# Kernel optimization log

Hardware: AMD Instinct MI355X
Metric: run time of the kernel (lower is better)

## Reference

```python
import jax, jax.numpy as jnp
import numpy as np

EPS = 1e-12


def t5_layer_norm(x, w):
    # RMS norm without mean subtraction (T5 style)
    var = jnp.mean(x * x, axis=-1, keepdims=True)
    return w * (x * jax.lax.rsqrt(var + EPS))


def gether(h, a_simi, t_simi, adj):
    # h: [B,S,S,D]; a_simi/t_simi: [B,S]; adj: [B,S,S]
    diag = jnp.einsum('bssd->bsd', h)                 # h[b,l,l,:]
    h_adj = jnp.einsum('bld,blk->blkd', diag, adj)    # diag broadcast by adjacency
    h_y = h * t_simi[:, None, :, None]                # t_simi varies along axis 2
    h_x = h * a_simi[:, :, None, None]                # a_simi varies along axis 1
    h_left = jnp.pad(h_y, ((0, 0), (0, 0), (1, 0), (0, 0)))[:, :, :-1, :]
    h_right = jnp.pad(h_y, ((0, 0), (0, 0), (0, 1), (0, 0)))[:, :, 1:, :]
    h_up = jnp.pad(h_x, ((0, 0), (1, 0), (0, 0), (0, 0)))[:, :-1, :, :]
    h_down = jnp.pad(h_x, ((0, 0), (0, 1), (0, 0), (0, 0)))[:, 1:, :, :]
    return h + h_adj + h_left + h_right + h_up + h_down


def setup_inputs() -> dict:
    key = jax.random.key(0)
    ks = jax.random.split(key, 10)
    B, S, D_in, D_out = 8, 96, 768, 256
    table = jax.random.normal(ks[0], (B, S, S, D_in), dtype=jnp.float32)
    a_simi = jax.random.uniform(ks[1], (B, S), dtype=jnp.float32)
    t_simi = jax.random.uniform(ks[2], (B, S), dtype=jnp.float32)
    adj_matrix = jax.random.uniform(ks[3], (B, S, S), dtype=jnp.float32)
    s1 = 1.0 / np.sqrt(D_in)
    W1 = jax.random.uniform(ks[4], (D_in, D_in), jnp.float32, -s1, s1)
    b1 = jax.random.uniform(ks[5], (D_in,), jnp.float32, -s1, s1)
    g1 = jnp.ones((D_in,), jnp.float32)
    W2 = jax.random.uniform(ks[6], (D_in, D_out), jnp.float32, -s1, s1)
    b2 = jax.random.uniform(ks[7], (D_out,), jnp.float32, -s1, s1)
    g2 = jnp.ones((D_out,), jnp.float32)
    return {"table": table, "a_simi": a_simi, "t_simi": t_simi,
            "adj_matrix": adj_matrix, "W1": W1, "b1": b1, "g1": g1,
            "W2": W2, "b2": b2, "g2": g2}


def reference(table, a_simi, t_simi, adj_matrix, W1, b1, g1, W2, b2, g2):
    h0 = table
    h1 = gether(h0, a_simi, t_simi, adj_matrix)
    h1 = jax.nn.relu(t5_layer_norm((h1 + h0) @ W1 + b1, g1))
    h2 = gether(h1, a_simi, t_simi, adj_matrix)
    h2 = jax.nn.relu(t5_layer_norm((h2 + h1) @ W2 + b2, g2))
    return h2
```

## Files before the change

### kernel.cpp

```cpp
#include <hip/hip_runtime.h>

typedef __bf16 bf16;
typedef __bf16 bf16x4 __attribute__((ext_vector_type(4)));
typedef __bf16 bf16x8 __attribute__((ext_vector_type(8)));
typedef float f32x4 __attribute__((ext_vector_type(4)));
typedef float floatx4 __attribute__((ext_vector_type(4)));

#define S 96
#define DIN 768
#define DOUT 256
#define MROWS 73728

__device__ static inline void async16(const bf16* g, bf16* l) {
    __builtin_amdgcn_global_load_lds(
        (const __attribute__((address_space(1))) void*)g,
        (__attribute__((address_space(3))) void*)l,
        16, 0, 0);
}

__global__ __launch_bounds__(256) void k_cast(
    const float* __restrict__ in, bf16* __restrict__ out, long n)
{
    long i = ((long)blockIdx.x * 256 + threadIdx.x) * 8;
    long stride = (long)gridDim.x * 256 * 8;
    for (; i < n; i += stride) {
        f32x4 a = *(const f32x4*)&in[i];
        f32x4 b = *(const f32x4*)&in[i + 4];
        bf16x8 o;
#pragma unroll
        for (int j = 0; j < 4; ++j) { o[j] = (bf16)a[j]; o[4 + j] = (bf16)b[j]; }
        *(bf16x8*)&out[i] = o;
    }
}

__global__ __launch_bounds__(512, 2) void k_gemm1(
    const bf16* __restrict__ Xm, const bf16* __restrict__ WT,
    bf16* __restrict__ Y)
{
    constexpr int K = 768, N = 768;
    constexpr int NTILE = K / 64;
    __shared__ __align__(16) bf16 As[2][256 * 64];
    __shared__ __align__(16) bf16 Bs[2][256 * 64];
    int t = threadIdx.x;
    int wg = blockIdx.x;
    wg = (wg & 7) * (gridDim.x >> 3) + (wg >> 3);
    int colBase = (wg % 3) * 256;
    int rowBase = (wg / 3) * 256;
    int lane = t & 63, w = t >> 6;
    int quad = lane >> 4, l16 = lane & 15;
    int wr = w >> 2, wc = w & 3;

    floatx4 acc[8][4];
#pragma unroll
    for (int i = 0; i < 8; ++i)
#pragma unroll
        for (int j = 0; j < 4; ++j) acc[i][j] = (floatx4)0.f;

    int tr = t >> 3;
    int gc = (t & 7) ^ (tr & 7);
    const bf16* gA = Xm + (size_t)(rowBase + tr) * K + gc * 8;
    const bf16* gB = WT + (size_t)(colBase + tr) * K + gc * 8;
    int ldst = t * 8;

    auto stageA = [&](int b, int s, int kt) {
        async16(gA + (size_t)s * 64 * K + kt * 64, &As[b][s * 4096 + ldst]);
    };
    auto stageB = [&](int b, int s, int kt) {
        async16(gB + (size_t)s * 64 * K + kt * 64, &Bs[b][s * 4096 + ldst]);
    };

    stageB(0, 0, 0); stageB(0, 1, 0); stageB(0, 2, 0); stageB(0, 3, 0);
    stageA(0, 0, 0); stageA(0, 2, 0); stageA(0, 1, 0); stageA(0, 3, 0);
    asm volatile("s_waitcnt vmcnt(2)" ::: "memory");
    __builtin_amdgcn_s_barrier();

    int swz = l16 & 7;
    int cK0 = (quad ^ swz) * 8;
    int cK1 = ((quad + 4) ^ swz) * 8;

    for (int tt = 0; tt < NTILE; ++tt) {
        int cur = tt & 1;
        int nb = cur ^ 1;
        bool more = (tt + 1 < NTILE);
        const bf16* aB = &As[cur][(wr * 128 + l16) * 64];
        const bf16* bB = &Bs[cur][(wc * 64 + l16) * 64];
#pragma unroll
        for (int p = 0; p < 4; ++p) {
            const int ihalf = p & 1;
            const int co = (p >> 1) ? cK1 : cK0;
            bf16x8 af[4], bfr[4];
#pragma unroll
            for (int ii = 0; ii < 4; ++ii)
                af[ii] = *(const bf16x8*)(aB + (ihalf * 4 + ii) * 1024 + co);
#pragma unroll
            for (int j = 0; j < 4; ++j)
                bfr[j] = *(const bf16x8*)(bB + j * 1024 + co);
            if (more) {
                if (p == 0) { stageB(nb, 0, tt + 1); stageB(nb, 1, tt + 1); }
                if (p == 1) { stageB(nb, 2, tt + 1); stageB(nb, 3, tt + 1); }
                if (p == 2) { stageA(nb, 0, tt + 1); stageA(nb, 2, tt + 1); }
                if (p == 3) { stageA(nb, 1, tt + 1); stageA(nb, 3, tt + 1); }
            }
            __builtin_amdgcn_s_barrier();
            asm volatile("s_waitcnt lgkmcnt(0)" ::: "memory");
            __builtin_amdgcn_sched_barrier(0);
            __builtin_amdgcn_s_setprio(1);
#pragma unroll
            for (int ii = 0; ii < 4; ++ii)
#pragma unroll
                for (int j = 0; j < 4; ++j)
                    acc[ihalf * 4 + ii][j] = __builtin_amdgcn_mfma_f32_16x16x32_bf16(
                        af[ii], bfr[j], acc[ihalf * 4 + ii][j], 0, 0, 0);
            __builtin_amdgcn_s_setprio(0);
            if (p == 0) {
                if (more) asm volatile("s_waitcnt vmcnt(2)" ::: "memory");
                else      asm volatile("s_waitcnt vmcnt(0)" ::: "memory");
            }
            if (p == 3 && more) asm volatile("s_waitcnt vmcnt(2)" ::: "memory");
            __builtin_amdgcn_s_barrier();
        }
    }

#pragma unroll
    for (int i = 0; i < 8; ++i) {
#pragma unroll
        for (int r = 0; r < 4; ++r) {
            int row = rowBase + wr * 128 + i * 16 + quad * 4 + r;
            bf16* yp = Y + (size_t)row * N + colBase + wc * 64 + l16;
#pragma unroll
            for (int j = 0; j < 4; ++j)
                yp[j * 16] = (bf16)acc[i][j][r];
        }
    }
}

__global__ __launch_bounds__(256) void k_gn1(
    const bf16* __restrict__ P, const float* __restrict__ G1,
    const float* __restrict__ B1, const float* __restrict__ Asim,
    const float* __restrict__ Tsim, const float* __restrict__ Adj,
    bf16* __restrict__ O)
{
    __shared__ float adjs[S];
    __shared__ float ts[S];
    __shared__ float diagf[DIN];
    __shared__ float g1s[DIN];
    __shared__ float b1s[DIN];
    int bx = blockIdx.x;
    bx = (bx & 7) * (gridDim.x >> 3) + (bx >> 3);
    int b = bx / S, l = bx % S;
    int tid = threadIdx.x;
    long row0 = (long)(b * S + l) * S;
    for (int i = tid; i < DIN; i += 256) { g1s[i] = G1[i]; b1s[i] = B1[i]; }
    if (tid < S) {
        adjs[tid] = Adj[(b * S + l) * S + tid];
        ts[tid]   = Tsim[b * S + tid];
        bf16x8 dv = *(const bf16x8*)&P[(row0 + l) * DIN + tid * 8];
#pragma unroll
        for (int j = 0; j < 8; ++j) diagf[tid * 8 + j] = (float)dv[j];
    }
    float a_up = (l > 0)     ? Asim[b * S + l - 1] : 0.f;
    float a_dn = (l < S - 1) ? Asim[b * S + l + 1] : 0.f;
    long du = (l > 0)     ? -(long)S * DIN : 0;
    long dd = (l < S - 1) ?  (long)S * DIN : 0;
    __syncthreads();

    int lane = tid & 63, wv = tid >> 6;
    int k0 = blockIdx.y * (S / 2);
    for (int k = k0 + wv; k < k0 + S / 2; k += 4) {
        float tl = (k > 0)     ? ts[k - 1] : 0.f;
        float tr = (k < S - 1) ? ts[k + 1] : 0.f;
        long  dl = (k > 0)     ? -(long)DIN : 0;
        long  dr = (k < S - 1) ?  (long)DIN : 0;
        float aj = adjs[k];
        const bf16* prow = P + (row0 + k) * DIN;
        bf16* orow = O + (row0 + k) * DIN;
        float v[12];
        float ss = 0.f;
        {
            int col = lane * 8;
            const bf16* pc = prow + col;
            bf16x8 vc = *(const bf16x8*)pc;
            bf16x8 vl = *(const bf16x8*)(pc + dl);
            bf16x8 vr = *(const bf16x8*)(pc + dr);
            bf16x8 vu = *(const bf16x8*)(pc + du);
            bf16x8 vd = *(const bf16x8*)(pc + dd);
#pragma unroll
            for (int j = 0; j < 8; ++j) {
                float x = 2.f * (float)vc[j] + aj * diagf[col + j]
                        + tl * (float)vl[j] + tr * (float)vr[j]
                        + a_up * (float)vu[j] + a_dn * (float)vd[j]
                        + b1s[col + j];
                v[j] = x;
                ss += x * x;
            }
        }
        {
            int col = 512 + lane * 4;
            const bf16* pc = prow + col;
            bf16x4 vc = *(const bf16x4*)pc;
            bf16x4 vl = *(const bf16x4*)(pc + dl);
            bf16x4 vr = *(const bf16x4*)(pc + dr);
            bf16x4 vu = *(const bf16x4*)(pc + du);
            bf16x4 vd = *(const bf16x4*)(pc + dd);
#pragma unroll
            for (int j = 0; j < 4; ++j) {
                float x = 2.f * (float)vc[j] + aj * diagf[col + j]
                        + tl * (float)vl[j] + tr * (float)vr[j]
                        + a_up * (float)vu[j] + a_dn * (float)vd[j]
                        + b1s[col + j];
                v[8 + j] = x;
                ss += x * x;
            }
        }
        ss += __shfl_xor(ss, 1);
        ss += __shfl_xor(ss, 2);
        ss += __shfl_xor(ss, 4);
        ss += __shfl_xor(ss, 8);
        ss += __shfl_xor(ss, 16);
        ss += __shfl_xor(ss, 32);
        float inv = rsqrtf(ss * (1.f / DIN) + 1e-12f);
        {
            int col = lane * 8;
            bf16x8 o;
#pragma unroll
            for (int j = 0; j < 8; ++j) {
                float y = v[j] * g1s[col + j] * inv;
                o[j] = (bf16)(y > 0.f ? y : 0.f);
            }
            *(bf16x8*)&orow[col] = o;
        }
        {
            int col = 512 + lane * 4;
            bf16x4 o;
#pragma unroll
            for (int j = 0; j < 4; ++j) {
                float y = v[8 + j] * g1s[col + j] * inv;
                o[j] = (bf16)(y > 0.f ? y : 0.f);
            }
            *(bf16x4*)&orow[col] = o;
        }
    }
}

__global__ __launch_bounds__(256, 2) void k_gemm2(
    const bf16* __restrict__ Xm, const bf16* __restrict__ WT,
    bf16* __restrict__ Y)
{
    constexpr int K = 768, N = 256;
    constexpr int NT = K / 32;
    __shared__ __align__(16) bf16 As[3][128 * 32];
    __shared__ __align__(16) bf16 Bs[3][256 * 32];
    int t = threadIdx.x;
    int rowBase = blockIdx.x * 128;
    int lane = t & 63, w = t >> 6;
    int quad = lane >> 4, l16 = lane & 15;
    int wr = w >> 1, wc = w & 1;

    floatx4 acc[4][8];
#pragma unroll
    for (int i = 0; i < 4; ++i)
#pragma unroll
        for (int j = 0; j < 8; ++j) acc[i][j] = (floatx4)0.f;

    int chunk = (t & 3) ^ ((t >> 3) & 3);
    const bf16* gA = Xm + (size_t)(rowBase + (t >> 2)) * K + chunk * 8;
    const bf16* gB = WT + (size_t)(t >> 2) * K + chunk * 8;
    int l8 = t * 8;

    auto stage = [&](int buf, int kk) {
        async16(gA + kk, &As[buf][l8]);
        async16(gA + kk + 64 * K, &As[buf][l8 + 2048]);
        async16(gB + kk, &Bs[buf][l8]);
        async16(gB + kk + 64 * K, &Bs[buf][l8 + 2048]);
        async16(gB + kk + 128 * K, &Bs[buf][l8 + 4096]);
        async16(gB + kk + 192 * K, &Bs[buf][l8 + 6144]);
    };

    stage(0, 0);
    stage(1, 32);
    for (int tt = 0; tt < NT; ++tt) {
        if (tt + 1 < NT) asm volatile("s_waitcnt vmcnt(6)" ::: "memory");
        else             asm volatile("s_waitcnt vmcnt(0)" ::: "memory");
        __builtin_amdgcn_s_barrier();
        int cur = tt % 3;
        bf16x8 af[4], bfr[8];
#pragma unroll
        for (int i = 0; i < 4; ++i) {
            int ra = wr * 64 + i * 16 + l16;
            af[i] = *(const bf16x8*)&As[cur][ra * 32 + (quad ^ ((ra >> 1) & 3)) * 8];
        }
#pragma unroll
        for (int j = 0; j < 8; ++j) {
            int rb = wc * 128 + j * 16 + l16;
            bfr[j] = *(const bf16x8*)&Bs[cur][rb * 32 + (quad ^ ((rb >> 1) & 3)) * 8];
        }
        if (tt + 2 < NT) stage((tt + 2) % 3, (tt + 2) * 32);
#pragma unroll
        for (int i = 0; i < 4; ++i)
#pragma unroll
            for (int j = 0; j < 8; ++j)
                acc[i][j] = __builtin_amdgcn_mfma_f32_16x16x32_bf16(
                    af[i], bfr[j], acc[i][j], 0, 0, 0);
    }

#pragma unroll
    for (int i = 0; i < 4; ++i) {
#pragma unroll
        for (int r = 0; r < 4; ++r) {
            int row = rowBase + wr * 64 + i * 16 + quad * 4 + r;
            bf16* yp = Y + (size_t)row * N + wc * 128 + l16;
#pragma unroll
            for (int j = 0; j < 8; ++j)
                yp[j * 16] = (bf16)acc[i][j][r];
        }
    }
}

__global__ __launch_bounds__(256) void k_gn2(
    const bf16* __restrict__ P, const float* __restrict__ G2,
    const float* __restrict__ B2, const float* __restrict__ Asim,
    const float* __restrict__ Tsim, const float* __restrict__ Adj,
    float* __restrict__ O)
{
    __shared__ float adjs[S];
    __shared__ float ts[S];
    __shared__ float diagf[DOUT];
    __shared__ float g2s[DOUT];
    __shared__ float b2s[DOUT];
    int bx = blockIdx.x;
    bx = (bx & 7) * (gridDim.x >> 3) + (bx >> 3);
    int b = bx / S, l = bx % S;
    int tid = threadIdx.x;
    long row0 = (long)(b * S + l) * S;
    if (tid < DOUT) { g2s[tid] = G2[tid]; b2s[tid] = B2[tid]; }
    if (tid < S) {
        adjs[tid] = Adj[(b * S + l) * S + tid];
        ts[tid]   = Tsim[b * S + tid];
    }
    if (tid < 32) {
        bf16x8 dv = *(const bf16x8*)&P[(row0 + l) * DOUT + tid * 8];
#pragma unroll
        for (int j = 0; j < 8; ++j) diagf[tid * 8 + j] = (float)dv[j];
    }
    float a_up = (l > 0)     ? Asim[b * S + l - 1] : 0.f;
    float a_dn = (l < S - 1) ? Asim[b * S + l + 1] : 0.f;
    long du = (l > 0)     ? -(long)S * DOUT : 0;
    long dd = (l < S - 1) ?  (long)S * DOUT : 0;
    __syncthreads();

    int lane = tid & 63, wv = tid >> 6;
    int k0 = blockIdx.y * (S / 2);
    for (int k = k0 + wv; k < k0 + S / 2; k += 4) {
        float tl = (k > 0)     ? ts[k - 1] : 0.f;
        float tr = (k < S - 1) ? ts[k + 1] : 0.f;
        long  dl = (k > 0)     ? -(long)DOUT : 0;
        long  dr = (k < S - 1) ?  (long)DOUT : 0;
        float aj = adjs[k];
        const bf16* prow = P + (row0 + k) * DOUT;
        float* orow = O + (row0 + k) * DOUT;
        int col = lane * 4;
        const bf16* pc = prow + col;
        bf16x4 vc = *(const bf16x4*)pc;
        bf16x4 vl = *(const bf16x4*)(pc + dl);
        bf16x4 vr = *(const bf16x4*)(pc + dr);
        bf16x4 vu = *(const bf16x4*)(pc + du);
        bf16x4 vd = *(const bf16x4*)(pc + dd);
        float v[4];
        float ss = 0.f;
#pragma unroll
        for (int j = 0; j < 4; ++j) {
            float x = 2.f * (float)vc[j] + aj * diagf[col + j]
                    + tl * (float)vl[j] + tr * (float)vr[j]
                    + a_up * (float)vu[j] + a_dn * (float)vd[j]
                    + b2s[col + j];
            v[j] = x;
            ss += x * x;
        }
        ss += __shfl_xor(ss, 1);
        ss += __shfl_xor(ss, 2);
        ss += __shfl_xor(ss, 4);
        ss += __shfl_xor(ss, 8);
        ss += __shfl_xor(ss, 16);
        ss += __shfl_xor(ss, 32);
        float inv = rsqrtf(ss * (1.f / DOUT) + 1e-12f);
        f32x4 o;
#pragma unroll
        for (int j = 0; j < 4; ++j) {
            float y = v[j] * g2s[col + j] * inv;
            o[j] = y > 0.f ? y : 0.f;
        }
        *(f32x4*)&orow[col] = o;
    }
}

__global__ __launch_bounds__(256) void k_castT(
    const float* __restrict__ in, bf16* __restrict__ out, int R, int C)
{
    __shared__ float tile[32][33];
    int lx = threadIdx.x & 31, ly = threadIdx.x >> 5;
    int c0 = blockIdx.x * 32, r0 = blockIdx.y * 32;
#pragma unroll
    for (int k = 0; k < 4; ++k)
        tile[ly + 8 * k][lx] = in[(size_t)(r0 + ly + 8 * k) * C + c0 + lx];
    __syncthreads();
#pragma unroll
    for (int k = 0; k < 4; ++k)
        out[(size_t)(c0 + ly + 8 * k) * R + r0 + lx] = (bf16)tile[lx][ly + 8 * k];
}

extern "C" void kernel_launch(void* const* d_in, const int* in_sizes, int n_in,
                              void* d_out, int out_size, void* d_ws, size_t ws_size,
                              hipStream_t stream)
{
    const float* table = (const float*)d_in[0];
    const float* asim  = (const float*)d_in[1];
    const float* tsim  = (const float*)d_in[2];
    const float* adj   = (const float*)d_in[3];
    const float* W1    = (const float*)d_in[4];
    const float* b1    = (const float*)d_in[5];
    const float* g1    = (const float*)d_in[6];
    const float* W2    = (const float*)d_in[7];
    const float* b2    = (const float*)d_in[8];
    const float* g2    = (const float*)d_in[9];
    float* out = (float*)d_out;

    char* ws = (char*)d_ws;
    const size_t SZ_X = (size_t)MROWS * DIN * 2;
    bf16*  A    = (bf16*)ws;
    bf16*  Bb   = (bf16*)(ws + SZ_X);
    bf16*  W1T  = (bf16*)(ws + 2 * SZ_X);
    bf16*  W2T  = (bf16*)(ws + 2 * SZ_X + 1179648);

    k_castT<<<dim3(DIN / 32, DIN / 32), 256, 0, stream>>>(W1, W1T, DIN, DIN);
    k_castT<<<dim3(DOUT / 32, DIN / 32), 256, 0, stream>>>(W2, W2T, DIN, DOUT);

    k_cast<<<2048, 256, 0, stream>>>(table, A, (long)MROWS * DIN);
    k_gemm1<<<dim3((DIN / 256) * (MROWS / 256)), 512, 0, stream>>>(A, W1T, Bb);
    k_gn1<<<dim3(8 * S, 2), 256, 0, stream>>>(Bb, g1, b1, asim, tsim, adj, A);
    k_gemm2<<<MROWS / 128, 256, 0, stream>>>(A, W2T, Bb);
    k_gn2<<<dim3(8 * S, 2), 256, 0, stream>>>(Bb, g2, b2, asim, tsim, adj, out);
}
```

Measured before the change: 586.9 us.

## Fuse fp32-to-bf16 input cast into first GEMM's A-tile loading

Removes the standalone cast kernel and has gemm1 load fp32 table rows directly. Each tile is converted to bf16 in registers before being written into shared memory. This eliminates a full read-write pass over the large input and the separate bf16 buffer read. In exchange, A loads go through registers instead of async direct-to-LDS loads, which adds register pressure and a full vmcnt wait per K tile.

```diff
diff --git a/kernel.cpp b/kernel.cpp
--- a/kernel.cpp
+++ b/kernel.cpp
@@ -18,23 +18,8 @@
         16, 0, 0);
 }
 
-__global__ __launch_bounds__(256) void k_cast(
-    const float* __restrict__ in, bf16* __restrict__ out, long n)
-{
-    long i = ((long)blockIdx.x * 256 + threadIdx.x) * 8;
-    long stride = (long)gridDim.x * 256 * 8;
-    for (; i < n; i += stride) {
-        f32x4 a = *(const f32x4*)&in[i];
-        f32x4 b = *(const f32x4*)&in[i + 4];
-        bf16x8 o;
-#pragma unroll
-        for (int j = 0; j < 4; ++j) { o[j] = (bf16)a[j]; o[4 + j] = (bf16)b[j]; }
-        *(bf16x8*)&out[i] = o;
-    }
-}
-
 __global__ __launch_bounds__(512, 2) void k_gemm1(
-    const bf16* __restrict__ Xm, const bf16* __restrict__ WT,
+    const float* __restrict__ X0, const bf16* __restrict__ WT,
     bf16* __restrict__ Y)
 {
     constexpr int K = 768, N = 768;
@@ -58,21 +43,35 @@
 
     int tr = t >> 3;
     int gc = (t & 7) ^ (tr & 7);
-    const bf16* gA = Xm + (size_t)(rowBase + tr) * K + gc * 8;
-    const bf16* gB = WT + (size_t)(colBase + tr) * K + gc * 8;
+    const float* gA = X0 + (size_t)(rowBase + tr) * K + gc * 8;
+    const bf16*  gB = WT + (size_t)(colBase + tr) * K + gc * 8;
     int ldst = t * 8;
 
-    auto stageA = [&](int b, int s, int kt) {
-        async16(gA + (size_t)s * 64 * K + kt * 64, &As[b][s * 4096 + ldst]);
+    auto loadA = [&](int s, int kt, f32x4& lo, f32x4& hi) {
+        const float* p = gA + (size_t)s * 64 * K + (size_t)kt * 64;
+        lo = *(const f32x4*)p;
+        hi = *(const f32x4*)(p + 4);
+    };
+    auto writeA = [&](int b, int s, f32x4 lo, f32x4 hi) {
+        bf16x8 o;
+#pragma unroll
+        for (int j = 0; j < 4; ++j) { o[j] = (bf16)lo[j]; o[4 + j] = (bf16)hi[j]; }
+        *(bf16x8*)&As[b][s * 4096 + ldst] = o;
     };
     auto stageB = [&](int b, int s, int kt) {
         async16(gB + (size_t)s * 64 * K + kt * 64, &Bs[b][s * 4096 + ldst]);
     };
 
-    stageB(0, 0, 0); stageB(0, 1, 0); stageB(0, 2, 0); stageB(0, 3, 0);
-    stageA(0, 0, 0); stageA(0, 2, 0); stageA(0, 1, 0); stageA(0, 3, 0);
-    asm volatile("s_waitcnt vmcnt(2)" ::: "memory");
-    __builtin_amdgcn_s_barrier();
+    {
+        f32x4 aLo, aHi, bLo, bHi;
+        loadA(0, 0, aLo, aHi); loadA(1, 0, bLo, bHi);
+        stageB(0, 0, 0); stageB(0, 1, 0); stageB(0, 2, 0); stageB(0, 3, 0);
+        writeA(0, 0, aLo, aHi); writeA(0, 1, bLo, bHi);
+        loadA(2, 0, aLo, aHi); loadA(3, 0, bLo, bHi);
+        writeA(0, 2, aLo, aHi); writeA(0, 3, bLo, bHi);
+        asm volatile("s_waitcnt vmcnt(0)" ::: "memory");
+    }
+    __syncthreads();
 
     int swz = l16 & 7;
     int cK0 = (quad ^ swz) * 8;
@@ -84,6 +83,7 @@
         bool more = (tt + 1 < NTILE);
         const bf16* aB = &As[cur][(wr * 128 + l16) * 64];
         const bf16* bB = &Bs[cur][(wc * 64 + l16) * 64];
+        f32x4 aLo, aHi, bLo, bHi;
 #pragma unroll
         for (int p = 0; p < 4; ++p) {
             const int ihalf = p & 1;
@@ -96,10 +96,18 @@
             for (int j = 0; j < 4; ++j)
                 bfr[j] = *(const bf16x8*)(bB + j * 1024 + co);
             if (more) {
-                if (p == 0) { stageB(nb, 0, tt + 1); stageB(nb, 1, tt + 1); }
-                if (p == 1) { stageB(nb, 2, tt + 1); stageB(nb, 3, tt + 1); }
-                if (p == 2) { stageA(nb, 0, tt + 1); stageA(nb, 2, tt + 1); }
-                if (p == 3) { stageA(nb, 1, tt + 1); stageA(nb, 3, tt + 1); }
+                if (p == 0) {
+                    loadA(0, tt + 1, aLo, aHi); loadA(1, tt + 1, bLo, bHi);
+                    stageB(nb, 0, tt + 1); stageB(nb, 1, tt + 1);
+                    stageB(nb, 2, tt + 1); stageB(nb, 3, tt + 1);
+                }
+                if (p == 1) {
+                    writeA(nb, 0, aLo, aHi); writeA(nb, 1, bLo, bHi);
+                    loadA(2, tt + 1, aLo, aHi); loadA(3, tt + 1, bLo, bHi);
+                }
+                if (p == 2) {
+                    writeA(nb, 2, aLo, aHi); writeA(nb, 3, bLo, bHi);
+                }
             }
             __builtin_amdgcn_s_barrier();
             asm volatile("s_waitcnt lgkmcnt(0)" ::: "memory");
@@ -112,11 +120,8 @@
                     acc[ihalf * 4 + ii][j] = __builtin_amdgcn_mfma_f32_16x16x32_bf16(
                         af[ii], bfr[j], acc[ihalf * 4 + ii][j], 0, 0, 0);
             __builtin_amdgcn_s_setprio(0);
-            if (p == 0) {
-                if (more) asm volatile("s_waitcnt vmcnt(2)" ::: "memory");
-                else      asm volatile("s_waitcnt vmcnt(0)" ::: "memory");
-            }
-            if (p == 3 && more) asm volatile("s_waitcnt vmcnt(2)" ::: "memory");
+            if (p == 3)
+                asm volatile("s_waitcnt vmcnt(0)" ::: "memory");
             __builtin_amdgcn_s_barrier();
         }
     }
@@ -434,8 +439,7 @@
     k_castT<<<dim3(DIN / 32, DIN / 32), 256, 0, stream>>>(W1, W1T, DIN, DIN);
     k_castT<<<dim3(DOUT / 32, DIN / 32), 256, 0, stream>>>(W2, W2T, DIN, DOUT);
 
-    k_cast<<<2048, 256, 0, stream>>>(table, A, (long)MROWS * DIN);
-    k_gemm1<<<dim3((DIN / 256) * (MROWS / 256)), 512, 0, stream>>>(A, W1T, Bb);
+    k_gemm1<<<dim3((DIN / 256) * (MROWS / 256)), 512, 0, stream>>>(table, W1T, Bb);
     k_gn1<<<dim3(8 * S, 2), 256, 0, stream>>>(Bb, g1, b1, asim, tsim, adj, A);
     k_gemm2<<<MROWS / 128, 256, 0, stream>>>(A, W2T, Bb);
     k_gn2<<<dim3(8 * S, 2), 256, 0, stream>>>(Bb, g2, b2, asim, tsim, adj, out);
```

Result: no change. 593.9 us (+1.2%).
